# Optimization experiments

Measured on AMD Instinct MI355X. Metric: run time of the kernel, lower is better.

Reference implementation:

```python
import jax, jax.numpy as jnp
import numpy as np
from jax import lax

EQN, GR = 10, 4
N, C, H, W = 8, 64, 16, 16


def _build_a(h, w):
    num = h * w
    a = np.zeros((num, EQN, 4 * num), np.float32)
    for i in range(num):
        right = (i + 1) % w != 0 and i + 1 < num
        down = i + w < num
        if right:
            a[i, 0, 2 * num + i] = 1.0; a[i, 0, i + 1] = -1.0
            a[i, 2, 2 * num + i] = 1.0; a[i, 2, 2 * num + i + 1] = -1.0
            a[i, 4, i] = 1.0;           a[i, 4, i + 1] = -1.0
            a[i, 6, 3 * num + i] = 1.0; a[i, 6, 3 * num + i + 1] = -1.0
            a[i, 8, num + i] = 1.0;     a[i, 8, num + i + 1] = -1.0
        if down:
            a[i, 1, 3 * num + i] = 1.0; a[i, 1, num + i + w] = -1.0
            a[i, 3, 3 * num + i] = 1.0; a[i, 3, 3 * num + i + w] = -1.0
            a[i, 5, num + i] = 1.0;     a[i, 5, num + i + w] = -1.0
            a[i, 7, 2 * num + i] = 1.0; a[i, 7, 2 * num + i + w] = -1.0
            a[i, 9, i] = 1.0;           a[i, 9, i + w] = -1.0
    last = num - 1
    a[last, 0, 2 * num + last] = 1.0
    a[last, 1, 3 * num + last] = 1.0
    a[last, 2, 2 * num + last] = 1.0
    a[last, 3, 3 * num + last] = 1.0
    a[last, 4, last] = 1.0
    a[last, 5, num + last] = 1.0
    a[last, 6, 3 * num + last] = 1.0
    a[last, 7, 2 * num + last] = 1.0
    a[last, 8, num + last] = 1.0
    a[last, 9, last] = 1.0
    return jnp.asarray(a)


def _conv(x, w, b):
    y = lax.conv_general_dilated(x, w, (1, 1), 'SAME',
                                 dimension_numbers=('NCHW', 'OIHW', 'NCHW'))
    return y + b[None, :, None, None]


def _lrelu(v):
    return jnp.where(v >= 0, v, 0.01 * v)


def setup_inputs() -> dict:
    key = jax.random.key(0)
    ks = jax.random.split(key, 18)
    s = 0.05
    d = {
        'x':   jax.random.normal(ks[0], (N, C, H, W), jnp.float32),
        'a':   _build_a(H, W),
        'gw1': jax.random.normal(ks[1], (C, C, 3, 3), jnp.float32) * s,
        'gb1': jnp.zeros((C,), jnp.float32),
        'gw2': jax.random.normal(ks[2], (EQN * GR, C, 3, 3), jnp.float32) * s,
        'gb2': jnp.zeros((EQN * GR,), jnp.float32),
        'aw1': jax.random.normal(ks[3], (C, C, 3, 3), jnp.float32) * s,
        'ab1': jnp.zeros((C,), jnp.float32),
        'aw2': jax.random.normal(ks[4], (EQN * GR, C, 3, 3), jnp.float32) * s,
        'ab2': jnp.zeros((EQN * GR,), jnp.float32),
        'sw1': jax.random.normal(ks[5], (C // 2, C, 1, 1), jnp.float32) * s,
        'sb1': jnp.zeros((C // 2,), jnp.float32),
        'sw2': jax.random.normal(ks[6], (4 * GR, C // 2, 1, 1), jnp.float32) * s,
        'sb2': jnp.zeros((4 * GR,), jnp.float32),
        'ins_w': jnp.ones((4 * GR,), jnp.float32),
        'ins_b': jnp.zeros((4 * GR,), jnp.float32),
        'pw':  jax.random.normal(ks[7], (128, 4 * GR, 3, 3), jnp.float32) * s,
        'pb':  jnp.zeros((128,), jnp.float32),
    }
    return d


def reference(x, a, gw1, gb1, gw2, gb2, aw1, ab1, aw2, ab2,
              sw1, sb1, sw2, sb2, ins_w, ins_b, pw, pb):
    n, c, h, w = x.shape
    num = h * w
    # attention / gradient / squeeze-excite branches
    att = jax.nn.sigmoid(_conv(_lrelu(_conv(x, aw1, ab1)), aw2, ab2))   # (n, eqn*gr, h, w)
    g   = _conv(_lrelu(_conv(x, gw1, gb1)), gw2, gb2)                   # (n, eqn*gr, h, w)
    pooled = x.mean(axis=(2, 3), keepdims=True)
    se = jax.nn.sigmoid(_conv(_lrelu(_conv(pooled, sw1, sb1)), sw2, sb2))  # (n, 4*gr, 1, 1)
    # reshape channels (gr, eqn), flatten batch*group, move pixel axis first
    att_r = att.reshape(n * GR, EQN, num).transpose(0, 2, 1)   # (ng, num, eqn)
    g_r   = g.reshape(n * GR, EQN, num).transpose(0, 2, 1)
    # weighted flow-equation system (done for all ng at once; the torch chunked
    # loop is only a memory optimization, math is identical)
    A = (a[None] * att_r[..., None]).reshape(n * GR, num * EQN, 4 * num)
    B = (g_r * att_r).reshape(n * GR, num * EQN)
    ATA = jnp.einsum('bki,bkj->bij', A, A)          # (ng, 4num, 4num)
    ATB = jnp.einsum('bki,bk->bi', A, B)            # (ng, 4num)
    ATA = ATA + jnp.eye(4 * num, dtype=x.dtype) * 1e-12
    sol = jnp.linalg.solve(ATA, ATB[..., None])     # (ng, 4num, 1)
    y = sol.reshape(n, 4 * GR, h, w)
    # GroupNorm(1, 4*gr): normalize over (C,H,W) per sample, per-channel affine
    mu = y.mean(axis=(1, 2, 3), keepdims=True)
    var = ((y - mu) ** 2).mean(axis=(1, 2, 3), keepdims=True)
    y = (y - mu) / jnp.sqrt(var + 1e-5)
    y = y * ins_w[None, :, None, None] + ins_b[None, :, None, None]
    y = se * y
    return _conv(y, pw, pb)
```

## Files before the change

### kernel.cpp

```cpp
#include <hip/hip_runtime.h>
#include <hip/hip_bf16.h>


#define NIT 48

__global__ __launch_bounds__(256) void k_se(
    const float* __restrict__ x, const float* __restrict__ sw1,
    const float* __restrict__ sb1, const float* __restrict__ sw2,
    const float* __restrict__ sb2, float* __restrict__ se)
{
  int n = blockIdx.x, t = threadIdx.x;
  __shared__ float part[64*4];
  __shared__ float pooled[64];
  __shared__ float h1[32];
  int c = t >> 2, q = t & 3;
  const float* xp = x + ((n*64 + c)*256) + q*64;
  float s = 0.f;
  #pragma unroll 8
  for (int j = 0; j < 64; ++j) s += xp[j];
  part[c*4+q] = s;
  __syncthreads();
  if (t < 64) pooled[t] = (part[t*4+0]+part[t*4+1]+part[t*4+2]+part[t*4+3]) * (1.f/256.f);
  __syncthreads();
  if (t < 32) {
    float a = sb1[t];
    for (int c2 = 0; c2 < 64; ++c2) a = fmaf(sw1[t*64+c2], pooled[c2], a);
    h1[t] = a >= 0.f ? a : 0.01f*a;
  }
  __syncthreads();
  if (t < 16) {
    float a = sb2[t];
    for (int c2 = 0; c2 < 32; ++c2) a = fmaf(sw2[t*32+c2], h1[c2], a);
    se[n*16+t] = 1.f/(1.f+__expf(-a));
  }
}

__device__ __forceinline__ float lane_bcast(float v, int src){
  return __int_as_float(__builtin_amdgcn_readlane(__float_as_int(v), src));
}

template<int CO_T, int CO_TOTAL, int ACT>
__global__ __launch_bounds__(512) void k_convw(
    const float* __restrict__ xg, const float* __restrict__ xa,
    const float* __restrict__ wg, const float* __restrict__ bg,
    const float* __restrict__ wa, const float* __restrict__ ba,
    float* __restrict__ outg, float* __restrict__ outa)
{
  const int tiles = CO_TOTAL / CO_T;
  int b = blockIdx.x;
  int tile = b % tiles; int rem = b / tiles;
  int br = rem & 1;     int n = rem >> 1;
  const float* xin  = br ? xa : xg;
  const float* w    = br ? wa : wg;
  const float* bias = br ? ba : bg;
  float* outp       = br ? outa : outg;
  int co_base = tile * CO_T;
  int t = threadIdx.x;
  int pp = t & 127, qc = t >> 7;
  int pr2 = pp >> 4, pc = pp & 15;
  int px0 = pr2*32 + pc, px1 = px0 + 16;
  int lane = t & 63;
  int cib = qc*16;
  __shared__ float xs[64*324];
  __shared__ float part[3][CO_T][256];
  int cil = cib + (lane & 15);
  float wv[CO_T*9];
  #pragma unroll
  for (int co = 0; co < CO_T; ++co) {
    const float* wp = w + ((size_t)(co_base+co)*64 + cil)*9;
    #pragma unroll
    for (int k = 0; k < 9; ++k) wv[co*9+k] = wp[k];
  }
  const float* xn = xin + (size_t)n*64*256;
  for (int idx = t; idx < 64*324; idx += 512) {
    int ch = idx / 324;
    int rm = idx - ch*324;
    int rr = rm / 18, cc = rm - rr*18;
    int sr = rr - 1, sc = cc - 1;
    float v = 0.f;
    if ((unsigned)sr < 16u && (unsigned)sc < 16u)
      v = xn[ch*256 + sr*16 + sc];
    xs[idx] = v;
  }
  __syncthreads();
  float accA[CO_T], accB[CO_T];
  #pragma unroll
  for (int co = 0; co < CO_T; ++co) { accA[co] = 0.f; accB[co] = 0.f; }
  #pragma unroll
  for (int ci = 0; ci < 16; ++ci) {
    const float* xr = xs + (cib+ci)*324 + (2*pr2)*18 + pc;
    float v0 = xr[0],  v1 = xr[1],  v2 = xr[2];
    float v3 = xr[18], v4 = xr[19], v5 = xr[20];
    float v6 = xr[36], v7 = xr[37], v8 = xr[38];
    float v9 = xr[54], v10 = xr[55], v11 = xr[56];
    #pragma unroll
    for (int co = 0; co < CO_T; ++co) {
      float w0 = lane_bcast(wv[co*9+0], ci);
      float w1 = lane_bcast(wv[co*9+1], ci);
      float w2 = lane_bcast(wv[co*9+2], ci);
      float w3 = lane_bcast(wv[co*9+3], ci);
      float w4 = lane_bcast(wv[co*9+4], ci);
      float w5 = lane_bcast(wv[co*9+5], ci);
      float w6 = lane_bcast(wv[co*9+6], ci);
      float w7 = lane_bcast(wv[co*9+7], ci);
      float w8 = lane_bcast(wv[co*9+8], ci);
      float aA = accA[co];
      aA = fmaf(v0,w0,aA); aA = fmaf(v1,w1,aA); aA = fmaf(v2,w2,aA);
      aA = fmaf(v3,w3,aA); aA = fmaf(v4,w4,aA); aA = fmaf(v5,w5,aA);
      aA = fmaf(v6,w6,aA); aA = fmaf(v7,w7,aA); aA = fmaf(v8,w8,aA);
      accA[co] = aA;
      float aB = accB[co];
      aB = fmaf(v3,w0,aB); aB = fmaf(v4,w1,aB); aB = fmaf(v5,w2,aB);
      aB = fmaf(v6,w3,aB); aB = fmaf(v7,w4,aB); aB = fmaf(v8,w5,aB);
      aB = fmaf(v9,w6,aB); aB = fmaf(v10,w7,aB); aB = fmaf(v11,w8,aB);
      accB[co] = aB;
    }
  }
  if (qc > 0) {
    #pragma unroll
    for (int co = 0; co < CO_T; ++co) {
      part[qc-1][co][px0] = accA[co];
      part[qc-1][co][px1] = accB[co];
    }
  }
  __syncthreads();
  if (qc == 0) {
    float* ob = outp + ((size_t)n*CO_TOTAL + co_base)*256;
    #pragma unroll
    for (int co = 0; co < CO_T; ++co) {
      float bsv = bias[co_base+co];
      float vA = bsv + accA[co] + part[0][co][px0] + part[1][co][px0] + part[2][co][px0];
      float vB = bsv + accB[co] + part[0][co][px1] + part[1][co][px1] + part[2][co][px1];
      if (ACT == 1) { vA = vA >= 0.f ? vA : 0.01f*vA; vB = vB >= 0.f ? vB : 0.01f*vB; }
      if (ACT == 2 && br) { vA = 1.f/(1.f+__expf(-vA)); vB = 1.f/(1.f+__expf(-vB)); }
      ob[co*256 + px0] = vA;
      ob[co*256 + px1] = vB;
    }
  }
}

__device__ __forceinline__ float wave_sum(float x){
  x += __int_as_float(__builtin_amdgcn_update_dpp(0, __float_as_int(x), 0x111, 0xf, 0xf, true));
  x += __int_as_float(__builtin_amdgcn_update_dpp(0, __float_as_int(x), 0x112, 0xf, 0xf, true));
  x += __int_as_float(__builtin_amdgcn_update_dpp(0, __float_as_int(x), 0x114, 0xf, 0xf, true));
  x += __int_as_float(__builtin_amdgcn_update_dpp(0, __float_as_int(x), 0x118, 0xf, 0xf, true));
  x += __int_as_float(__builtin_amdgcn_update_dpp(0, __float_as_int(x), 0x142, 0xa, 0xf, true));
  x += __int_as_float(__builtin_amdgcn_update_dpp(0, __float_as_int(x), 0x143, 0xc, 0xf, true));
  return __int_as_float(__builtin_amdgcn_readlane(__float_as_int(x), 63));
}
__device__ __forceinline__ float dpp_prev(float v){
  return __int_as_float(__builtin_amdgcn_update_dpp(0, __float_as_int(v), 0x138, 0xf, 0xf, true));
}
__device__ __forceinline__ float dpp_next(float v){
  return __int_as_float(__builtin_amdgcn_update_dpp(0, __float_as_int(v), 0x130, 0xf, 0xf, true));
}

__global__ __launch_bounds__(64, 1) void k_cg(
    const float* __restrict__ att, const float* __restrict__ gm,
    float* __restrict__ yout)
{
  int bg = blockIdx.x;
  int n = bg >> 2, g = bg & 3;
  const float* ab = att + ((size_t)n*40 + g*10)*256;
  const float* gb = gm  + ((size_t)n*40 + g*10)*256;
  __shared__ float sbuf[10][256];
  __shared__ float tbuf[10][256];
  __shared__ float pl[4][256];
  int l = threadIdx.x;
  int base = l*4;
  int rI = l >> 2;
  int c0 = (l & 3)*4;
  bool rU4 = (rI > 0), hD4 = (rI < 15);
  int iL0 = (base > 0) ? base-1 : 0;
  int iUc = rU4 ? base-16 : base;
  int iDc = hD4 ? base+16 : base;

  float sr[10][4], tr[10][4];
  #pragma unroll
  for (int e = 0; e < 10; ++e) {
    float4 av = *(const float4*)(ab + e*256 + base);
    float4 gv = *(const float4*)(gb + e*256 + base);
    sr[e][0]=av.x*av.x; sr[e][1]=av.y*av.y; sr[e][2]=av.z*av.z; sr[e][3]=av.w*av.w;
    tr[e][0]=sr[e][0]*gv.x; tr[e][1]=sr[e][1]*gv.y; tr[e][2]=sr[e][2]*gv.z; tr[e][3]=sr[e][3]*gv.w;
    *(float4*)(&sbuf[e][base]) = make_float4(sr[e][0],sr[e][1],sr[e][2],sr[e][3]);
    *(float4*)(&tbuf[e][base]) = make_float4(tr[e][0],tr[e][1],tr[e][2],tr[e][3]);
  }
  __syncthreads();

  const int eL[5] = {0,2,4,6,8};
  const int eU[5] = {1,3,5,7,9};
  float sLs[5][4], tLs[5][4], sUs[5][4], tUs[5][4];
  float gU = rU4 ? 1.f : 0.f;
  #pragma unroll
  for (int k = 0; k < 5; ++k) {
    int e = eL[k];
    sLs[k][0] = (c0 > 0) ? sbuf[e][iL0] : 0.f;
    tLs[k][0] = (c0 > 0) ? tbuf[e][iL0] : 0.f;
    #pragma unroll
    for (int j = 1; j < 4; ++j) { sLs[k][j] = sr[e][j-1]; tLs[k][j] = tr[e][j-1]; }
  }
  #pragma unroll
  for (int k = 0; k < 5; ++k) {
    int e = eU[k];
    float4 su = *(const float4*)(&sbuf[e][iUc]);
    float4 tu = *(const float4*)(&tbuf[e][iUc]);
    sUs[k][0]=su.x*gU; sUs[k][1]=su.y*gU; sUs[k][2]=su.z*gU; sUs[k][3]=su.w*gU;
    tUs[k][0]=tu.x*gU; tUs[k][1]=tu.y*gU; tUs[k][2]=tu.z*gU; tUs[k][3]=tu.w*gU;
  }

  float k0R[4],k0L[4],k0X[4],k0D[4],k0U[4], d0[4],di0[4], b0[4];
  float k1R[4],k1L[4],k1D[4],k1U[4],k1X[4], d1[4],di1[4], b1[4];
  float k2R[4],k2L[4],k2D[4],k2U[4],k2X[4], d2[4],di2[4], b2[4];
  float k3R[4],k3L[4],k3D[4],k3U[4],k3X[4], d3[4],di3[4], b3[4];
  #pragma unroll
  for (int j = 0; j < 4; ++j) {
    bool hR = (c0 + j) < 15;
    bool hD = hD4;
    bool last = (l == 63) && (j == 3);
    k0R[j] = hR ? sr[4][j] : 0.f;  k0L[j] = sLs[2][j];  k0X[j] = sLs[0][j];
    k0D[j] = hD ? sr[9][j] : 0.f;  k0U[j] = sUs[4][j];
    k1R[j] = hR ? sr[8][j] : 0.f;  k1L[j] = sLs[4][j];
    k1D[j] = hD ? sr[5][j] : 0.f;  k1U[j] = sUs[2][j];  k1X[j] = sUs[0][j];
    k2R[j] = hR ? sr[2][j] : 0.f;  k2L[j] = sLs[1][j];
    k2D[j] = hD ? sr[7][j] : 0.f;  k2U[j] = sUs[3][j];  k2X[j] = hR ? sr[0][j] : 0.f;
    k3R[j] = hR ? sr[6][j] : 0.f;  k3L[j] = sLs[3][j];
    k3D[j] = hD ? sr[3][j] : 0.f;  k3U[j] = sUs[1][j];  k3X[j] = hD ? sr[1][j] : 0.f;
    d0[j] = k0R[j]+k0L[j]+k0X[j]+k0D[j]+k0U[j] + (last ? sr[4][j]+sr[9][j] : 0.f);
    d1[j] = k1R[j]+k1L[j]+k1D[j]+k1U[j]+k1X[j] + (last ? sr[5][j]+sr[8][j] : 0.f);
    d2[j] = k2R[j]+k2L[j]+k2D[j]+k2U[j]+k2X[j] + (last ? sr[0][j]+sr[2][j]+sr[7][j] : 0.f);
    d3[j] = k3R[j]+k3L[j]+k3D[j]+k3U[j]+k3X[j] + (last ? sr[1][j]+sr[3][j]+sr[6][j] : 0.f);
    b0[j] = (hR?tr[4][j]:0.f) - tLs[2][j] - tLs[0][j] + (hD?tr[9][j]:0.f) - tUs[4][j]
          + (last ? tr[4][j]+tr[9][j] : 0.f);
    b1[j] = (hR?tr[8][j]:0.f) - tLs[4][j] + (hD?tr[5][j]:0.f) - tUs[2][j] - tUs[0][j]
          + (last ? tr[5][j]+tr[8][j] : 0.f);
    b2[j] = (hR?(tr[2][j]+tr[0][j]):0.f) - tLs[1][j] + (hD?tr[7][j]:0.f) - tUs[3][j]
          + (last ? tr[0][j]+tr[2][j]+tr[7][j] : 0.f);
    b3[j] = (hR?tr[6][j]:0.f) - tLs[3][j] + (hD?(tr[3][j]+tr[1][j]):0.f) - tUs[1][j]
          + (last ? tr[1][j]+tr[3][j]+tr[6][j] : 0.f);
    di0[j] = 1.f/(d0[j]+1e-20f); di1[j] = 1.f/(d1[j]+1e-20f);
    di2[j] = 1.f/(d2[j]+1e-20f); di3[j] = 1.f/(d3[j]+1e-20f);
  }

  float vA = sr[0][3]+sr[2][3]+sr[4][3]+sr[7][3]+sr[9][3];
  float vB = sr[1][3]+sr[3][3]+sr[5][3]+sr[6][3]+sr[8][3];
  float ei1 = 1.f/(__shfl(vA, 63, 64)+1e-20f);
  float ei2 = 1.f/(__shfl(vB, 63, 64)+1e-20f);

  float x0[4],x1[4],x2[4],x3[4], r0[4],r1[4],r2[4],r3[4], p0[4],p1[4],p2[4],p3[4];
  float rdr_p = 0.f, ca_p = 0.f, cb_p = 0.f;
  #pragma unroll
  for (int j = 0; j < 4; ++j) {
    x0[j]=0.f; x1[j]=0.f; x2[j]=0.f; x3[j]=0.f;
    r0[j]=b0[j]; r1[j]=b1[j]; r2[j]=b2[j]; r3[j]=b3[j];
    rdr_p += r0[j]*r0[j]*di0[j] + r1[j]*r1[j]*di1[j] + r2[j]*r2[j]*di2[j] + r3[j]*r3[j]*di3[j];
    ca_p += r0[j]+r2[j]; cb_p += r1[j]+r3[j];
  }
  float rdr = wave_sum(rdr_p), ca = wave_sum(ca_p), cb = wave_sum(cb_p);
  float rz = rdr + ca*ca*ei1 + cb*cb*ei2;
  float cc1 = ca*ei1, cc2 = cb*ei2;
  #pragma unroll
  for (int j = 0; j < 4; ++j) {
    p0[j] = di0[j]*r0[j] + cc1; p1[j] = di1[j]*r1[j] + cc2;
    p2[j] = di2[j]*r2[j] + cc1; p3[j] = di3[j]*r3[j] + cc2;
  }
  *(float4*)(&pl[0][base]) = make_float4(p0[0],p0[1],p0[2],p0[3]);
  *(float4*)(&pl[1][base]) = make_float4(p1[0],p1[1],p1[2],p1[3]);
  *(float4*)(&pl[2][base]) = make_float4(p2[0],p2[1],p2[2],p2[3]);
  *(float4*)(&pl[3][base]) = make_float4(p3[0],p3[1],p3[2],p3[3]);
  __syncthreads();

  for (int it = 0; it < NIT; ++it) {
    float nR0 = dpp_next(p0[0]), nR1 = dpp_next(p1[0]),
          nR2 = dpp_next(p2[0]), nR3 = dpp_next(p3[0]);
    float nL0 = dpp_prev(p0[3]), nL1 = dpp_prev(p1[3]),
          nL2 = dpp_prev(p2[3]), nL3 = dpp_prev(p3[3]);
    float4 u0 = *(const float4*)(&pl[0][iUc]);
    float4 u1 = *(const float4*)(&pl[1][iUc]);
    float4 u2 = *(const float4*)(&pl[2][iUc]);
    float4 u3 = *(const float4*)(&pl[3][iUc]);
    float4 w0 = *(const float4*)(&pl[0][iDc]);
    float4 w1 = *(const float4*)(&pl[1][iDc]);
    float4 w2 = *(const float4*)(&pl[2][iDc]);
    float4 w3 = *(const float4*)(&pl[3][iDc]);
    float pU0[4]={u0.x,u0.y,u0.z,u0.w}, pU1[4]={u1.x,u1.y,u1.z,u1.w};
    float pU2[4]={u2.x,u2.y,u2.z,u2.w}, pU3[4]={u3.x,u3.y,u3.z,u3.w};
    float pD0[4]={w0.x,w0.y,w0.z,w0.w}, pD1[4]={w1.x,w1.y,w1.z,w1.w};
    float pD2[4]={w2.x,w2.y,w2.z,w2.w}, pD3[4]={w3.x,w3.y,w3.z,w3.w};
    float q0[4],q1[4],q2[4],q3[4];
    float pq_p = 0.f;
    #pragma unroll
    for (int j = 0; j < 4; ++j) {
      float p0R = (j<3)? p0[j+1] : nR0;  float p0L = (j>0)? p0[j-1] : nL0;
      float p1R = (j<3)? p1[j+1] : nR1;  float p1L = (j>0)? p1[j-1] : nL1;
      float p2R = (j<3)? p2[j+1] : nR2;  float p2L = (j>0)? p2[j-1] : nL2;
      float p3R = (j<3)? p3[j+1] : nR3;  float p3L = (j>0)? p3[j-1] : nL3;
      q0[j] = d0[j]*p0[j] - k0R[j]*p0R - k0L[j]*p0L - k0X[j]*p2L - k0D[j]*pD0[j] - k0U[j]*pU0[j];
      q1[j] = d1[j]*p1[j] - k1R[j]*p1R - k1L[j]*p1L - k1D[j]*pD1[j] - k1U[j]*pU1[j] - k1X[j]*pU3[j];
      q2[j] = d2[j]*p2[j] - k2R[j]*p2R - k2L[j]*p2L - k2D[j]*pD2[j] - k2U[j]*pU2[j] - k2X[j]*p0R;
      q3[j] = d3[j]*p3[j] - k3R[j]*p3R - k3L[j]*p3L - k3D[j]*pD3[j] - k3U[j]*pU3[j] - k3X[j]*pD1[j];
      pq_p += p0[j]*q0[j] + p1[j]*q1[j] + p2[j]*q2[j] + p3[j]*q3[j];
    }
    float pq = wave_sum(pq_p);
    float alpha = pq > 1e-35f ? rz/pq : 0.f;
    float rdr2_p = 0.f, ca2_p = 0.f, cb2_p = 0.f;
    #pragma unroll
    for (int j = 0; j < 4; ++j) {
      x0[j] = fmaf(alpha,p0[j],x0[j]); x1[j] = fmaf(alpha,p1[j],x1[j]);
      x2[j] = fmaf(alpha,p2[j],x2[j]); x3[j] = fmaf(alpha,p3[j],x3[j]);
      r0[j] = fmaf(-alpha,q0[j],r0[j]); r1[j] = fmaf(-alpha,q1[j],r1[j]);
      r2[j] = fmaf(-alpha,q2[j],r2[j]); r3[j] = fmaf(-alpha,q3[j],r3[j]);
      rdr2_p += r0[j]*r0[j]*di0[j] + r1[j]*r1[j]*di1[j] + r2[j]*r2[j]*di2[j] + r3[j]*r3[j]*di3[j];
      ca2_p += r0[j]+r2[j]; cb2_p += r1[j]+r3[j];
    }
    float rdrT = wave_sum(rdr2_p), c1T = wave_sum(ca2_p), c2T = wave_sum(cb2_p);
    float rz2 = rdrT + c1T*c1T*ei1 + c2T*c2T*ei2;
    float beta = rz > 1e-35f ? rz2/rz : 0.f;
    rz = rz2;
    float z1c = c1T*ei1, z2c = c2T*ei2;
    #pragma unroll
    for (int j = 0; j < 4; ++j) {
      p0[j] = fmaf(beta,p0[j], di0[j]*r0[j] + z1c);
      p1[j] = fmaf(beta,p1[j], di1[j]*r1[j] + z2c);
      p2[j] = fmaf(beta,p2[j], di2[j]*r2[j] + z1c);
      p3[j] = fmaf(beta,p3[j], di3[j]*r3[j] + z2c);
    }
    *(float4*)(&pl[0][base]) = make_float4(p0[0],p0[1],p0[2],p0[3]);
    *(float4*)(&pl[1][base]) = make_float4(p1[0],p1[1],p1[2],p1[3]);
    *(float4*)(&pl[2][base]) = make_float4(p2[0],p2[1],p2[2],p2[3]);
    *(float4*)(&pl[3][base]) = make_float4(p3[0],p3[1],p3[2],p3[3]);
    __syncthreads();
  }
  float* yo = yout + ((size_t)n*16 + g*4)*256 + base;
  *(float4*)(yo)       = make_float4(x0[0],x0[1],x0[2],x0[3]);
  *(float4*)(yo + 256) = make_float4(x1[0],x1[1],x1[2],x1[3]);
  *(float4*)(yo + 512) = make_float4(x2[0],x2[1],x2[2],x2[3]);
  *(float4*)(yo + 768) = make_float4(x3[0],x3[1],x3[2],x3[3]);
}

template<int CO_T>
__global__ __launch_bounds__(256) void k_out(
    const float* __restrict__ y, const float* __restrict__ insw,
    const float* __restrict__ insb, const float* __restrict__ sev,
    const float* __restrict__ pw, const float* __restrict__ pb,
    float* __restrict__ out)
{
  const int tiles = 128 / CO_T;
  int b = blockIdx.x;
  int cot = b % tiles, n = b / tiles;
  int co_base = cot * CO_T;
  int t = threadIdx.x;
  int pr = t >> 4, pc = t & 15;
  __shared__ float ys[16*324];
  __shared__ float wl[CO_T*16*12];
  __shared__ float redA[4], redB[4];
  const float* yb = y + (size_t)n*16*256;
  float s = 0.f, s2 = 0.f;
  #pragma unroll
  for (int c = 0; c < 16; ++c) {
    float v = yb[c*256 + t];
    s += v; s2 = fmaf(v, v, s2);
  }
  for (int idx = t; idx < CO_T*144; idx += 256) {
    int co = idx / 144; int rm = idx - co*144;
    int ci = rm / 9; int k = rm - ci*9;
    wl[(co*16 + ci)*12 + k] = pw[(size_t)(co_base+co)*144 + rm];
  }
  for (int idx = t; idx < 16*324; idx += 256) {
    int ch = idx / 324;
    int rem = idx - ch*324;
    int rr = rem / 18, cc = rem - rr*18;
    int sr = rr-1, sc = cc-1;
    float v = 0.f;
    if ((unsigned)sr < 16u && (unsigned)sc < 16u) v = yb[ch*256 + sr*16 + sc];
    ys[idx] = v;
  }
  int lane = t & 63, wid = t >> 6;
  #pragma unroll
  for (int m = 1; m < 64; m <<= 1) { s += __shfl_xor(s, m, 64); s2 += __shfl_xor(s2, m, 64); }
  if (lane == 0) { redA[wid] = s; redB[wid] = s2; }
  __syncthreads();
  float S  = redA[0]+redA[1]+redA[2]+redA[3];
  float SS = redB[0]+redB[1]+redB[2]+redB[3];
  float mu = S * (1.f/4096.f);
  float var = SS * (1.f/4096.f) - mu*mu;
  float rstd = rsqrtf(var + 1e-5f);
  for (int idx = t; idx < 16*324; idx += 256) {
    int ch = idx / 324;
    int rem = idx - ch*324;
    int rr = rem / 18, cc = rem - rr*18;
    int sr = rr-1, sc = cc-1;
    if ((unsigned)sr < 16u && (unsigned)sc < 16u) {
      float sef = sev[n*16+ch];
      float m = rstd * insw[ch] * sef;
      float a = (insb[ch] - mu*rstd*insw[ch]) * sef;
      ys[idx] = fmaf(ys[idx], m, a);
    }
  }
  __syncthreads();
  float acc[CO_T];
  #pragma unroll
  for (int co = 0; co < CO_T; ++co) acc[co] = pb[co_base+co];
  for (int ci = 0; ci < 16; ++ci) {
    const float* xr = ys + ci*324 + pr*18 + pc;
    float x0 = xr[0],  x1 = xr[1],  x2 = xr[2];
    float x3 = xr[18], x4 = xr[19], x5 = xr[20];
    float x6 = xr[36], x7 = xr[37], x8 = xr[38];
    #pragma unroll
    for (int co = 0; co < CO_T; ++co) {
      const float4* wv = ((const float4*)wl) + (co*16 + ci)*3;
      float4 wa = wv[0], wb = wv[1], wc = wv[2];
      float a = acc[co];
      a = fmaf(x0,wa.x,a); a = fmaf(x1,wa.y,a); a = fmaf(x2,wa.z,a);
      a = fmaf(x3,wa.w,a); a = fmaf(x4,wb.x,a); a = fmaf(x5,wb.y,a);
      a = fmaf(x6,wb.z,a); a = fmaf(x7,wb.w,a); a = fmaf(x8,wc.x,a);
      acc[co] = a;
    }
  }
  float* ob = out + ((size_t)n*128 + co_base)*256 + t;
  #pragma unroll
  for (int co = 0; co < CO_T; ++co)
    ob[co*256] = acc[co];
}

extern "C" void kernel_launch(void* const* d_in, const int* in_sizes, int n_in,
                              void* d_out, int out_size, void* d_ws, size_t ws_size,
                              hipStream_t stream) {
  const float* x    = (const float*)d_in[0];
  const float* gw1  = (const float*)d_in[2];
  const float* gb1  = (const float*)d_in[3];
  const float* gw2  = (const float*)d_in[4];
  const float* gb2  = (const float*)d_in[5];
  const float* aw1  = (const float*)d_in[6];
  const float* ab1  = (const float*)d_in[7];
  const float* aw2  = (const float*)d_in[8];
  const float* ab2  = (const float*)d_in[9];
  const float* sw1  = (const float*)d_in[10];
  const float* sb1  = (const float*)d_in[11];
  const float* sw2  = (const float*)d_in[12];
  const float* sb2  = (const float*)d_in[13];
  const float* insw = (const float*)d_in[14];
  const float* insb = (const float*)d_in[15];
  const float* pw   = (const float*)d_in[16];
  const float* pb   = (const float*)d_in[17];
  float* ws = (float*)d_ws;
  float* g1   = ws;
  float* a1   = ws + 131072;
  float* gmat = ws + 262144;
  float* attb = ws + 344064;
  float* sev  = ws + 425984;
  float* ybuf = ws + 426112;
  float* out  = (float*)d_out;

  k_se<<<dim3(8), dim3(256), 0, stream>>>(x, sw1, sb1, sw2, sb2, sev);
  k_convw<4,64,1><<<dim3(256), dim3(512), 0, stream>>>(x, x, gw1, gb1, aw1, ab1, g1, a1);
  k_convw<4,40,2><<<dim3(160), dim3(512), 0, stream>>>(g1, a1, gw2, gb2, aw2, ab2, gmat, attb);
  k_cg<<<dim3(32), dim3(64), 0, stream>>>(attb, gmat, ybuf);
  k_out<4><<<dim3(256), dim3(256), 0, stream>>>(ybuf, insw, insb, sev, pw, pb, out);
}
```

Baseline: 89.83 us.

## Restructure preconditioned CG into single-reduction Chronopoulos-Gear form

```diff
diff --git a/kernel.cpp b/kernel.cpp
--- a/kernel.cpp
+++ b/kernel.cpp
@@ -243,91 +243,99 @@
 
   float vA = sr[0][3]+sr[2][3]+sr[4][3]+sr[7][3]+sr[9][3];
   float vB = sr[1][3]+sr[3][3]+sr[5][3]+sr[6][3]+sr[8][3];
-  float ei1 = 1.f/(__shfl(vA, 63, 64)+1e-20f);
-  float ei2 = 1.f/(__shfl(vB, 63, 64)+1e-20f);
-
-  float x0[4],x1[4],x2[4],x3[4], r0[4],r1[4],r2[4],r3[4], p0[4],p1[4],p2[4],p3[4];
-  float rdr_p = 0.f, ca_p = 0.f, cb_p = 0.f;
+  float vAb = lane_bcast(vA, 63);
+  float vBb = lane_bcast(vB, 63);
+  float ei1 = 1.f/(vAb+1e-20f), ei2 = 1.f/(vBb+1e-20f);
+  float m63 = (l == 63) ? 1.f : 0.f;
+  float eA0 = m63*(sr[4][3]+sr[9][3]);
+  float eA2 = m63*(sr[0][3]+sr[2][3]+sr[7][3]);
+  float eB1 = m63*(sr[5][3]+sr[8][3]);
+  float eB3 = m63*(sr[1][3]+sr[3][3]+sr[6][3]);
+
+  float x0[4],x1[4],x2[4],x3[4], r0[4],r1[4],r2[4],r3[4];
+  float p0[4],p1[4],p2[4],p3[4], s0[4],s1[4],s2[4],s3[4];
   #pragma unroll
   for (int j = 0; j < 4; ++j) {
     x0[j]=0.f; x1[j]=0.f; x2[j]=0.f; x3[j]=0.f;
     r0[j]=b0[j]; r1[j]=b1[j]; r2[j]=b2[j]; r3[j]=b3[j];
-    rdr_p += r0[j]*r0[j]*di0[j] + r1[j]*r1[j]*di1[j] + r2[j]*r2[j]*di2[j] + r3[j]*r3[j]*di3[j];
-    ca_p += r0[j]+r2[j]; cb_p += r1[j]+r3[j];
-  }
-  float rdr = wave_sum(rdr_p), ca = wave_sum(ca_p), cb = wave_sum(cb_p);
-  float rz = rdr + ca*ca*ei1 + cb*cb*ei2;
-  float cc1 = ca*ei1, cc2 = cb*ei2;
-  #pragma unroll
-  for (int j = 0; j < 4; ++j) {
-    p0[j] = di0[j]*r0[j] + cc1; p1[j] = di1[j]*r1[j] + cc2;
-    p2[j] = di2[j]*r2[j] + cc1; p3[j] = di3[j]*r3[j] + cc2;
-  }
-  *(float4*)(&pl[0][base]) = make_float4(p0[0],p0[1],p0[2],p0[3]);
-  *(float4*)(&pl[1][base]) = make_float4(p1[0],p1[1],p1[2],p1[3]);
-  *(float4*)(&pl[2][base]) = make_float4(p2[0],p2[1],p2[2],p2[3]);
-  *(float4*)(&pl[3][base]) = make_float4(p3[0],p3[1],p3[2],p3[3]);
-  __syncthreads();
+    p0[j]=0.f; p1[j]=0.f; p2[j]=0.f; p3[j]=0.f;
+    s0[j]=0.f; s1[j]=0.f; s2[j]=0.f; s3[j]=0.f;
+  }
+  float gamma_old = 1.f, alpha_old = 1.f;
 
   for (int it = 0; it < NIT; ++it) {
-    float nR0 = dpp_next(p0[0]), nR1 = dpp_next(p1[0]),
-          nR2 = dpp_next(p2[0]), nR3 = dpp_next(p3[0]);
-    float nL0 = dpp_prev(p0[3]), nL1 = dpp_prev(p1[3]),
-          nL2 = dpp_prev(p2[3]), nL3 = dpp_prev(p3[3]);
-    float4 u0 = *(const float4*)(&pl[0][iUc]);
-    float4 u1 = *(const float4*)(&pl[1][iUc]);
-    float4 u2 = *(const float4*)(&pl[2][iUc]);
-    float4 u3 = *(const float4*)(&pl[3][iUc]);
-    float4 w0 = *(const float4*)(&pl[0][iDc]);
-    float4 w1 = *(const float4*)(&pl[1][iDc]);
-    float4 w2 = *(const float4*)(&pl[2][iDc]);
-    float4 w3 = *(const float4*)(&pl[3][iDc]);
-    float pU0[4]={u0.x,u0.y,u0.z,u0.w}, pU1[4]={u1.x,u1.y,u1.z,u1.w};
-    float pU2[4]={u2.x,u2.y,u2.z,u2.w}, pU3[4]={u3.x,u3.y,u3.z,u3.w};
-    float pD0[4]={w0.x,w0.y,w0.z,w0.w}, pD1[4]={w1.x,w1.y,w1.z,w1.w};
-    float pD2[4]={w2.x,w2.y,w2.z,w2.w}, pD3[4]={w3.x,w3.y,w3.z,w3.w};
-    float q0[4],q1[4],q2[4],q3[4];
-    float pq_p = 0.f;
+    float u0[4],u1[4],u2[4],u3[4];
     #pragma unroll
     for (int j = 0; j < 4; ++j) {
-      float p0R = (j<3)? p0[j+1] : nR0;  float p0L = (j>0)? p0[j-1] : nL0;
-      float p1R = (j<3)? p1[j+1] : nR1;  float p1L = (j>0)? p1[j-1] : nL1;
-      float p2R = (j<3)? p2[j+1] : nR2;  float p2L = (j>0)? p2[j-1] : nL2;
-      float p3R = (j<3)? p3[j+1] : nR3;  float p3L = (j>0)? p3[j-1] : nL3;
-      q0[j] = d0[j]*p0[j] - k0R[j]*p0R - k0L[j]*p0L - k0X[j]*p2L - k0D[j]*pD0[j] - k0U[j]*pU0[j];
-      q1[j] = d1[j]*p1[j] - k1R[j]*p1R - k1L[j]*p1L - k1D[j]*pD1[j] - k1U[j]*pU1[j] - k1X[j]*pU3[j];
-      q2[j] = d2[j]*p2[j] - k2R[j]*p2R - k2L[j]*p2L - k2D[j]*pD2[j] - k2U[j]*pU2[j] - k2X[j]*p0R;
-      q3[j] = d3[j]*p3[j] - k3R[j]*p3R - k3L[j]*p3L - k3D[j]*pD3[j] - k3U[j]*pU3[j] - k3X[j]*pD1[j];
-      pq_p += p0[j]*q0[j] + p1[j]*q1[j] + p2[j]*q2[j] + p3[j]*q3[j];
-    }
-    float pq = wave_sum(pq_p);
-    float alpha = pq > 1e-35f ? rz/pq : 0.f;
-    float rdr2_p = 0.f, ca2_p = 0.f, cb2_p = 0.f;
+      u0[j]=di0[j]*r0[j]; u1[j]=di1[j]*r1[j];
+      u2[j]=di2[j]*r2[j]; u3[j]=di3[j]*r3[j];
+    }
+    *(float4*)(&pl[0][base]) = make_float4(u0[0],u0[1],u0[2],u0[3]);
+    *(float4*)(&pl[1][base]) = make_float4(u1[0],u1[1],u1[2],u1[3]);
+    *(float4*)(&pl[2][base]) = make_float4(u2[0],u2[1],u2[2],u2[3]);
+    *(float4*)(&pl[3][base]) = make_float4(u3[0],u3[1],u3[2],u3[3]);
+    __syncthreads();
+    float nR0 = dpp_next(u0[0]), nR1 = dpp_next(u1[0]),
+          nR2 = dpp_next(u2[0]), nR3 = dpp_next(u3[0]);
+    float nL0 = dpp_prev(u0[3]), nL1 = dpp_prev(u1[3]),
+          nL2 = dpp_prev(u2[3]), nL3 = dpp_prev(u3[3]);
+    float4 uu0 = *(const float4*)(&pl[0][iUc]);
+    float4 uu1 = *(const float4*)(&pl[1][iUc]);
+    float4 uu2 = *(const float4*)(&pl[2][iUc]);
+    float4 uu3 = *(const float4*)(&pl[3][iUc]);
+    float4 dd0 = *(const float4*)(&pl[0][iDc]);
+    float4 dd1 = *(const float4*)(&pl[1][iDc]);
+    float4 dd2 = *(const float4*)(&pl[2][iDc]);
+    float4 dd3 = *(const float4*)(&pl[3][iDc]);
+    float uU0[4]={uu0.x,uu0.y,uu0.z,uu0.w}, uU1[4]={uu1.x,uu1.y,uu1.z,uu1.w};
+    float uU2[4]={uu2.x,uu2.y,uu2.z,uu2.w}, uU3[4]={uu3.x,uu3.y,uu3.z,uu3.w};
+    float uD0[4]={dd0.x,dd0.y,dd0.z,dd0.w}, uD1[4]={dd1.x,dd1.y,dd1.z,dd1.w};
+    float uD2[4]={dd2.x,dd2.y,dd2.z,dd2.w}, uD3[4]={dd3.x,dd3.y,dd3.z,dd3.w};
+    float w0[4],w1[4],w2[4],w3[4];
+    float rDr=0.f, SA=0.f, SB=0.f, uw=0.f, TA=0.f, TB=0.f;
     #pragma unroll
     for (int j = 0; j < 4; ++j) {
-      x0[j] = fmaf(alpha,p0[j],x0[j]); x1[j] = fmaf(alpha,p1[j],x1[j]);
-      x2[j] = fmaf(alpha,p2[j],x2[j]); x3[j] = fmaf(alpha,p3[j],x3[j]);
-      r0[j] = fmaf(-alpha,q0[j],r0[j]); r1[j] = fmaf(-alpha,q1[j],r1[j]);
-      r2[j] = fmaf(-alpha,q2[j],r2[j]); r3[j] = fmaf(-alpha,q3[j],r3[j]);
-      rdr2_p += r0[j]*r0[j]*di0[j] + r1[j]*r1[j]*di1[j] + r2[j]*r2[j]*di2[j] + r3[j]*r3[j]*di3[j];
-      ca2_p += r0[j]+r2[j]; cb2_p += r1[j]+r3[j];
-    }
-    float rdrT = wave_sum(rdr2_p), c1T = wave_sum(ca2_p), c2T = wave_sum(cb2_p);
-    float rz2 = rdrT + c1T*c1T*ei1 + c2T*c2T*ei2;
-    float beta = rz > 1e-35f ? rz2/rz : 0.f;
-    rz = rz2;
-    float z1c = c1T*ei1, z2c = c2T*ei2;
+      float a0R = (j<3)? u0[j+1] : nR0;  float a0L = (j>0)? u0[j-1] : nL0;
+      float a1R = (j<3)? u1[j+1] : nR1;  float a1L = (j>0)? u1[j-1] : nL1;
+      float a2R = (j<3)? u2[j+1] : nR2;  float a2L = (j>0)? u2[j-1] : nL2;
+      float a3R = (j<3)? u3[j+1] : nR3;  float a3L = (j>0)? u3[j-1] : nL3;
+      w0[j] = d0[j]*u0[j] - k0R[j]*a0R - k0L[j]*a0L - k0X[j]*a2L - k0D[j]*uD0[j] - k0U[j]*uU0[j];
+      w1[j] = d1[j]*u1[j] - k1R[j]*a1R - k1L[j]*a1L - k1D[j]*uD1[j] - k1U[j]*uU1[j] - k1X[j]*uU3[j];
+      w2[j] = d2[j]*u2[j] - k2R[j]*a2R - k2L[j]*a2L - k2D[j]*uD2[j] - k2U[j]*uU2[j] - k2X[j]*a0R;
+      w3[j] = d3[j]*u3[j] - k3R[j]*a3R - k3L[j]*a3L - k3D[j]*uD3[j] - k3U[j]*uU3[j] - k3X[j]*uD1[j];
+      rDr += r0[j]*u0[j] + r1[j]*u1[j] + r2[j]*u2[j] + r3[j]*u3[j];
+      SA  += r0[j]+r2[j];  SB += r1[j]+r3[j];
+      uw  += u0[j]*w0[j] + u1[j]*w1[j] + u2[j]*w2[j] + u3[j]*w3[j];
+      TA  += w0[j]+w2[j];  TB += w1[j]+w3[j];
+    }
+    float uaA = lane_bcast(u0[3]*eA0 + u2[3]*eA2, 63);
+    float uaB = lane_bcast(u1[3]*eB1 + u3[3]*eB3, 63);
+    rDr = wave_sum(rDr); SA = wave_sum(SA); SB = wave_sum(SB);
+    uw  = wave_sum(uw);  TA = wave_sum(TA); TB = wave_sum(TB);
+    float c1 = SA*ei1, c2 = SB*ei2;
+    float gamma = rDr + SA*c1 + SB*c2;
+    float delta = uw + c1*(uaA + TA) + c2*(uaB + TB) + c1*c1*vAb + c2*c2*vBb;
+    float beta  = (it == 0) ? 0.f : gamma/gamma_old;
+    float denom = delta - beta*(gamma/alpha_old);
+    float alpha = (fabsf(denom) > 1e-30f) ? gamma/denom : 0.f;
+    w0[3] = fmaf(c1, eA0, w0[3]);  w2[3] = fmaf(c1, eA2, w2[3]);
+    w1[3] = fmaf(c2, eB1, w1[3]);  w3[3] = fmaf(c2, eB3, w3[3]);
     #pragma unroll
     for (int j = 0; j < 4; ++j) {
-      p0[j] = fmaf(beta,p0[j], di0[j]*r0[j] + z1c);
-      p1[j] = fmaf(beta,p1[j], di1[j]*r1[j] + z2c);
-      p2[j] = fmaf(beta,p2[j], di2[j]*r2[j] + z1c);
-      p3[j] = fmaf(beta,p3[j], di3[j]*r3[j] + z2c);
-    }
-    *(float4*)(&pl[0][base]) = make_float4(p0[0],p0[1],p0[2],p0[3]);
-    *(float4*)(&pl[1][base]) = make_float4(p1[0],p1[1],p1[2],p1[3]);
-    *(float4*)(&pl[2][base]) = make_float4(p2[0],p2[1],p2[2],p2[3]);
-    *(float4*)(&pl[3][base]) = make_float4(p3[0],p3[1],p3[2],p3[3]);
+      p0[j] = fmaf(beta, p0[j], u0[j] + c1);
+      p1[j] = fmaf(beta, p1[j], u1[j] + c2);
+      p2[j] = fmaf(beta, p2[j], u2[j] + c1);
+      p3[j] = fmaf(beta, p3[j], u3[j] + c2);
+      s0[j] = fmaf(beta, s0[j], w0[j]);
+      s1[j] = fmaf(beta, s1[j], w1[j]);
+      s2[j] = fmaf(beta, s2[j], w2[j]);
+      s3[j] = fmaf(beta, s3[j], w3[j]);
+      x0[j] = fmaf(alpha, p0[j], x0[j]); x1[j] = fmaf(alpha, p1[j], x1[j]);
+      x2[j] = fmaf(alpha, p2[j], x2[j]); x3[j] = fmaf(alpha, p3[j], x3[j]);
+      r0[j] = fmaf(-alpha, s0[j], r0[j]); r1[j] = fmaf(-alpha, s1[j], r1[j]);
+      r2[j] = fmaf(-alpha, s2[j], r2[j]); r3[j] = fmaf(-alpha, s3[j], r3[j]);
+    }
+    gamma_old = gamma; alpha_old = alpha;
     __syncthreads();
   }
   float* yo = yout + ((size_t)n*16 + g*4)*256 + base;
```

New measurement: 105.2 us. 17.1% more time.
